# Kernel optimization log

Hardware: AMD Instinct MI355X
Metric: run time of the kernel (lower is better)

Reference implementation:

```python
import jax, jax.numpy as jnp
import numpy as np

B, S, HID = 4, 1024, 2048
NH, NKV = 32, 8
HD = HID // NH  # 64
N_REP = NH // NKV
THETA = 10000.0


def _rope_cos_sin(position_ids, head_dim, dtype):
    inv_freq = 1.0 / (THETA ** (jnp.arange(0, head_dim, 2, dtype=jnp.float32) / head_dim))
    ang = position_ids.astype(jnp.float32)[:, None] * inv_freq[None, :]  # [S, HD/2]
    emb = jnp.concatenate([ang, ang], axis=-1)  # [S, HD]
    return jnp.cos(emb).astype(dtype), jnp.sin(emb).astype(dtype)


def _rotate_half(x):
    x1, x2 = jnp.split(x, 2, axis=-1)
    return jnp.concatenate([-x2, x1], axis=-1)


def setup_inputs() -> dict:
    key = jax.random.key(0)
    ks = jax.random.split(key, 6)
    scale = 0.02
    hidden_states = jax.random.normal(ks[0], (B, S, HID), dtype=jnp.float32)
    # causal additive mask
    neg = jnp.finfo(jnp.float32).min
    causal = jnp.where(jnp.tril(jnp.ones((S, S), dtype=bool)), 0.0, neg)
    attention_mask = causal[None, None, :, :].astype(jnp.float32)
    position_ids = jnp.arange(S, dtype=jnp.int32)
    Wq = jax.random.normal(ks[1], (HID, NH * HD), dtype=jnp.float32) * scale
    Wk = jax.random.normal(ks[2], (HID, NKV * HD), dtype=jnp.float32) * scale
    Wv = jax.random.normal(ks[3], (HID, NKV * HD), dtype=jnp.float32) * scale
    Wo = jax.random.normal(ks[4], (NH * HD, HID), dtype=jnp.float32) * scale
    return {"hidden_states": hidden_states, "attention_mask": attention_mask,
            "position_ids": position_ids, "Wq": Wq, "Wk": Wk, "Wv": Wv, "Wo": Wo}


def reference(hidden_states, attention_mask, position_ids, Wq, Wk, Wv, Wo):
    b, s, _ = hidden_states.shape
    dtype = hidden_states.dtype
    q = (hidden_states @ Wq).reshape(b, s, NH, HD).transpose(0, 2, 1, 3)   # [B,NH,S,HD]
    k = (hidden_states @ Wk).reshape(b, s, NKV, HD).transpose(0, 2, 1, 3)  # [B,NKV,S,HD]
    v = (hidden_states @ Wv).reshape(b, s, NKV, HD).transpose(0, 2, 1, 3)
    # RoPE
    cos, sin = _rope_cos_sin(position_ids, HD, dtype)  # [S,HD]
    cos = cos[None, None, :, :]
    sin = sin[None, None, :, :]
    q = q * cos + _rotate_half(q) * sin
    k = k * cos + _rotate_half(k) * sin
    # repeat KV heads to match query heads
    k = jnp.repeat(k, N_REP, axis=1)  # [B,NH,S,HD]
    v = jnp.repeat(v, N_REP, axis=1)
    scale = HD ** -0.5
    attn = jnp.einsum('bhqd,bhkd->bhqk', q, k) * scale + attention_mask
    attn = jax.nn.softmax(attn.astype(jnp.float32), axis=-1).astype(dtype)
    out = jnp.einsum('bhqk,bhkd->bhqd', attn, v)  # [B,NH,S,HD]
    out = out.transpose(0, 2, 1, 3).reshape(b, s, NH * HD)
    return out @ Wo
```

## Files before the change

### kernel.cpp

```cpp
#include <hip/hip_runtime.h>
#include <hip/hip_bf16.h>
#include <math.h>

typedef __bf16 bf16_t;
typedef __bf16 bf16x4 __attribute__((ext_vector_type(4)));
typedef __bf16 bf16x8 __attribute__((ext_vector_type(8)));
typedef float f32x4 __attribute__((ext_vector_type(4)));

#define MFMA_BF16(a, b, c) __builtin_amdgcn_mfma_f32_16x16x32_bf16((a), (b), (c), 0, 0, 0)

__device__ __forceinline__ void gload_lds16(const void* g, void* s) {
  __builtin_amdgcn_global_load_lds((const __attribute__((address_space(1))) void*)g,
                                   (__attribute__((address_space(3))) void*)s, 16, 0, 0);
}

__device__ __forceinline__ bf16x8 lds_frag(const bf16_t* base, int row, int k) {
  const char* p = reinterpret_cast<const char*>(base) + row * 128 + ((((k >> 3) ^ (row & 7)) << 4));
  return *reinterpret_cast<const bf16x8*>(p);
}

__global__ __launch_bounds__(256) void k_cvt_x(const float* __restrict__ X, bf16_t* __restrict__ Xb) {
  const int i = blockIdx.x * 256 + threadIdx.x;
  const float4* X4 = reinterpret_cast<const float4*>(X);
  const float4 a = X4[2 * i], c = X4[2 * i + 1];
  bf16x8 v;
  v[0] = (bf16_t)a.x; v[1] = (bf16_t)a.y; v[2] = (bf16_t)a.z; v[3] = (bf16_t)a.w;
  v[4] = (bf16_t)c.x; v[5] = (bf16_t)c.y; v[6] = (bf16_t)c.z; v[7] = (bf16_t)c.w;
  reinterpret_cast<bf16x8*>(Xb)[i] = v;
}

__global__ __launch_bounds__(256) void k_transpose(const float* __restrict__ W, bf16_t* __restrict__ Wt,
                                                   int K, int N) {
  __shared__ bf16_t t[64][65];
  const int k0 = blockIdx.y * 64, n0 = blockIdx.x * 64;
  const int tid = threadIdx.x;
#pragma unroll
  for (int i = 0; i < 16; ++i) {
    const int idx = i * 256 + tid;
    const int kl = idx >> 6, nl = idx & 63;
    t[nl][kl] = (bf16_t)W[(size_t)(k0 + kl) * N + n0 + nl];
  }
  __syncthreads();
#pragma unroll
  for (int i = 0; i < 16; ++i) {
    const int idx = i * 256 + tid;
    const int nl = idx >> 6, kl = idx & 63;
    Wt[(size_t)(n0 + nl) * K + k0 + kl] = t[nl][kl];
  }
}

__global__ __launch_bounds__(256) void k_transpose_qkv(const float* __restrict__ Wq,
                                                       const float* __restrict__ Wk,
                                                       const float* __restrict__ Wv,
                                                       bf16_t* __restrict__ Wt) {
  __shared__ bf16_t t[64][65];
  const int n0 = blockIdx.x * 64;
  const int k0 = blockIdx.y * 64;
  const int tid = threadIdx.x;
  const float* W;
  int N, nbase;
  if (n0 < 2048)      { W = Wq; N = 2048; nbase = 0; }
  else if (n0 < 2560) { W = Wk; N = 512;  nbase = 2048; }
  else                { W = Wv; N = 512;  nbase = 2560; }
  const int nl0 = n0 - nbase;
#pragma unroll
  for (int i = 0; i < 16; ++i) {
    const int idx = i * 256 + tid;
    const int kl = idx >> 6, nl = idx & 63;
    t[nl][kl] = (bf16_t)W[(size_t)(k0 + kl) * N + nl0 + nl];
  }
  __syncthreads();
#pragma unroll
  for (int i = 0; i < 16; ++i) {
    const int idx = i * 256 + tid;
    const int nl = idx >> 6, kl = idx & 63;
    Wt[(size_t)(n0 + nl) * 2048 + k0 + kl] = t[nl][kl];
  }
}

__global__ __launch_bounds__(512) void k_gemm_qkv(const bf16_t* __restrict__ A,
                                                  const bf16_t* __restrict__ Bt,
                                                  const int* __restrict__ pos_ids,
                                                  bf16_t* __restrict__ Qb,
                                                  bf16_t* __restrict__ Kb,
                                                  bf16_t* __restrict__ Vt) {
  constexpr int K = 2048;
  constexpr int NT = K / 64;
  __shared__ __align__(16) char smem[131072];
  const int tid = threadIdx.x;
  const int w = tid >> 6, l = tid & 63;
  const int wm = w >> 2, wn = w & 3;
  const int g = l >> 4, ln = l & 15;
  const int orig = blockIdx.y * 12 + blockIdx.x;
  const int swz = (orig & 7) * 24 + (orig >> 3);
  const int m0 = (swz / 12) * 256, n0 = (swz % 12) * 256;
  const int csrc = ((l & 7) ^ (l >> 3)) * 8;
  const int srow = w * 16 + (l >> 3);

  auto STAGE_A = [&](int slot, int h, int kt) {
    char* base = smem + slot * 32768 + h * 16384 + w * 2048;
    const bf16_t* gs = A + (size_t)(m0 + h * 128 + srow) * K + kt + csrc;
    gload_lds16(gs, base);
    gload_lds16(gs + (size_t)8 * K, base + 1024);
  };
  auto STAGE_B = [&](int slot, int h, int kt) {
    char* base = smem + 65536 + slot * 32768 + h * 16384 + w * 2048;
    const bf16_t* gs = Bt + (size_t)(n0 + h * 128 + srow) * K + kt + csrc;
    gload_lds16(gs, base);
    gload_lds16(gs + (size_t)8 * K, base + 1024);
  };
  auto FRAG = [&](const char* half, int row, int kk) -> bf16x8 {
    return *reinterpret_cast<const bf16x8*>(half + row * 128 + ((((kk >> 3) ^ (row & 7)) << 4)));
  };

  const f32x4 zero4 = {0.f, 0.f, 0.f, 0.f};
  f32x4 acc[8][4];
#pragma unroll
  for (int i = 0; i < 8; ++i)
#pragma unroll
    for (int j = 0; j < 4; ++j) acc[i][j] = zero4;

  STAGE_A(0, 0, 0); STAGE_A(0, 1, 0);
  STAGE_B(0, 0, 0); STAGE_B(0, 1, 0);
  STAGE_B(1, 0, 64); STAGE_B(1, 1, 64);
  asm volatile("s_waitcnt vmcnt(4)" ::: "memory");
  __builtin_amdgcn_sched_barrier(0);
  __builtin_amdgcn_s_barrier();
  __builtin_amdgcn_sched_barrier(0);

  const int rb = (wn & 1) * 64;
  for (int t = 0; t < NT; ++t) {
    const int s = t & 1;
    const char* Ah = smem + s * 32768 + wm * 16384;
    const char* Bh = smem + 65536 + s * 32768 + (wn >> 1) * 16384;
    bf16x8 bB[4][2];
#pragma unroll
    for (int q = 0; q < 4; ++q) {
      if (q == 0) {
#pragma unroll
        for (int fc = 0; fc < 4; ++fc)
#pragma unroll
          for (int kh = 0; kh < 2; ++kh) bB[fc][kh] = FRAG(Bh, rb + fc * 16 + ln, kh * 32 + g * 8);
      }
      bf16x8 aA[2][2];
#pragma unroll
      for (int e = 0; e < 2; ++e)
#pragma unroll
        for (int kh = 0; kh < 2; ++kh) aA[e][kh] = FRAG(Ah, (q * 2 + e) * 16 + ln, kh * 32 + g * 8);
      if (q == 0 && t + 1 < NT) STAGE_A(s ^ 1, 0, (t + 1) * 64);
      if (q == 1 && t + 1 < NT) STAGE_A(s ^ 1, 1, (t + 1) * 64);
      if (q == 2 && t + 2 < NT) STAGE_B(s, 0, (t + 2) * 64);
      if (q == 3 && t + 2 < NT) STAGE_B(s, 1, (t + 2) * 64);
      if (q == 3) {
        if (t >= NT - 2) asm volatile("s_waitcnt vmcnt(0)" ::: "memory");
        else             asm volatile("s_waitcnt vmcnt(4)" ::: "memory");
      }
      __builtin_amdgcn_sched_barrier(0);
      __builtin_amdgcn_s_barrier();
      __builtin_amdgcn_sched_barrier(0);
      __builtin_amdgcn_s_setprio(1);
#pragma unroll
      for (int e = 0; e < 2; ++e)
#pragma unroll
        for (int fc = 0; fc < 4; ++fc)
#pragma unroll
          for (int kh = 0; kh < 2; ++kh)
            acc[q * 2 + e][fc] = MFMA_BF16(aA[e][kh], bB[fc][kh], acc[q * 2 + e][fc]);
      __builtin_amdgcn_s_setprio(0);
      __builtin_amdgcn_sched_barrier(0);
      __builtin_amdgcn_s_barrier();
      __builtin_amdgcn_sched_barrier(0);
    }
  }

  const int colbase = n0 + wn * 64;
  const int rowbase = m0 + wm * 128;
  const float if0 = exp2f(-(float)ln * 0.4152410118609203f);
  const float if1 = exp2f(-(float)(ln + 16) * 0.4152410118609203f);
  const float QS = 0.125f * 1.4426950408889634f;

  if (colbase < 2560) {
    const bool isQ = (colbase < 2048);
    bf16_t* out = isQ ? (Qb + (size_t)(colbase >> 6) * 1024 * 64)
                      : (Kb + (size_t)((colbase - 2048) >> 6) * 1024 * 64);
    const size_t bstride = isQ ? (size_t)32 * 1024 * 64 : (size_t)8 * 1024 * 64;
    const float sc = isQ ? QS : 1.0f;
#pragma unroll
    for (int i = 0; i < 8; ++i)
#pragma unroll
      for (int r = 0; r < 4; ++r) {
        const int row = rowbase + i * 16 + g * 4 + r;
        const int b = row >> 10, s = row & 1023;
        const float pos = (float)pos_ids[s];
        float sn0, cs0, sn1, cs1;
        __sincosf(pos * if0, &sn0, &cs0);
        __sincosf(pos * if1, &sn1, &cs1);
        const float x0 = acc[i][0][r], x1 = acc[i][1][r];
        const float x2 = acc[i][2][r], x3 = acc[i][3][r];
        const float o0 = (x0 * cs0 - x2 * sn0) * sc;
        const float o2 = (x2 * cs0 + x0 * sn0) * sc;
        const float o1 = (x1 * cs1 - x3 * sn1) * sc;
        const float o3 = (x3 * cs1 + x1 * sn1) * sc;
        bf16_t* p = out + (size_t)b * bstride + (size_t)s * 64;
        p[ln] = (bf16_t)o0;
        p[16 + ln] = (bf16_t)o1;
        p[32 + ln] = (bf16_t)o2;
        p[48 + ln] = (bf16_t)o3;
      }
  } else {
    const int kh = (colbase - 2560) >> 6;
#pragma unroll
    for (int i = 0; i < 8; ++i)
#pragma unroll
      for (int r = 0; r < 4; ++r) {
        const int row = rowbase + i * 16 + g * 4 + r;
        const int b = row >> 10, s = row & 1023;
        const size_t vb = ((size_t)(b * 8 + kh) * 64) * 1024;
#pragma unroll
        for (int j = 0; j < 4; ++j) {
          const int d = j * 16 + ln;
          Vt[vb + (size_t)d * 1024 + s] = (bf16_t)acc[i][j][r];
        }
      }
  }
}

template <typename OutT>
__global__ __launch_bounds__(256) void k_gemm(const bf16_t* __restrict__ A,
                                              const bf16_t* __restrict__ Bt,
                                              OutT* __restrict__ C,
                                              int M, int N, int K) {
  __shared__ bf16_t As[128 * 64];
  __shared__ bf16_t Bs[128 * 64];
  const int tid = threadIdx.x;
  const int w = tid >> 6, l = tid & 63;
  const int nwgx = gridDim.x;
  const int orig = blockIdx.y * nwgx + blockIdx.x;
  const int cpx = (nwgx * gridDim.y) >> 3;
  const int swz = (orig & 7) * cpx + (orig >> 3);
  const int m0 = (swz / nwgx) * 128, n0 = (swz % nwgx) * 128;
  const int wr = (w >> 1) * 64, wc = (w & 1) * 64;
  const int g = l >> 4, ln = l & 15;
  const int lr = l >> 3;
  const int csrc = ((l & 7) ^ lr) * 8;

  const f32x4 zero4 = {0.f, 0.f, 0.f, 0.f};
  f32x4 acc[4][4];
#pragma unroll
  for (int i = 0; i < 4; ++i)
#pragma unroll
    for (int j = 0; j < 4; ++j) acc[i][j] = zero4;

  for (int kt = 0; kt < K; kt += 64) {
    __syncthreads();
#pragma unroll
    for (int c = 0; c < 4; ++c) {
      const int cq = c * 4 + w;
      const int r = cq * 8 + lr;
      gload_lds16(A + (size_t)(m0 + r) * K + kt + csrc, As + cq * 512);
      gload_lds16(Bt + (size_t)(n0 + r) * K + kt + csrc, Bs + cq * 512);
    }
    asm volatile("s_waitcnt vmcnt(0)" ::: "memory");
    __syncthreads();
#pragma unroll
    for (int ks = 0; ks < 2; ++ks) {
      bf16x8 af[4], bfv[4];
#pragma unroll
      for (int i = 0; i < 4; ++i) af[i] = lds_frag(As, wr + i * 16 + ln, ks * 32 + g * 8);
#pragma unroll
      for (int j = 0; j < 4; ++j) bfv[j] = lds_frag(Bs, wc + j * 16 + ln, ks * 32 + g * 8);
#pragma unroll
      for (int i = 0; i < 4; ++i)
#pragma unroll
        for (int j = 0; j < 4; ++j) acc[i][j] = MFMA_BF16(af[i], bfv[j], acc[i][j]);
    }
  }
#pragma unroll
  for (int i = 0; i < 4; ++i)
#pragma unroll
    for (int j = 0; j < 4; ++j)
#pragma unroll
      for (int r = 0; r < 4; ++r) {
        const int row = m0 + wr + i * 16 + g * 4 + r;
        const int col = n0 + wc + j * 16 + ln;
        C[(size_t)row * N + col] = (OutT)acc[i][j][r];
      }
}

__global__ __launch_bounds__(256) void k_attn(const bf16_t* __restrict__ Qb,
                                              const bf16_t* __restrict__ Kb,
                                              const bf16_t* __restrict__ Vt,
                                              bf16_t* __restrict__ AO) {
  __shared__ bf16_t Ks[2][64 * 64];
  __shared__ bf16_t Vs[2][64 * 64];
  __shared__ bf16_t Ps[4][16 * 64];
  const int tid = threadIdx.x;
  const int w = tid >> 6, l = tid & 63;
  const int g = l >> 4, ln = l & 15;
  const int lr = l >> 3;
  const int csrc = ((l & 7) ^ lr) * 8;
  const int f = blockIdx.x;
  const int bh = blockIdx.y;
  const int b = bh >> 5, h = bh & 31, kh = h >> 2;
  const int qA0 = f * 64, qB0 = (15 - f) * 64;
  const int qAw = qA0 + w * 16, qBw = qB0 + w * 16;
  const bf16_t* Qh = Qb + (size_t)(b * 32 + h) * 1024 * 64;
  const bf16_t* Kh = Kb + (size_t)(b * 8 + kh) * 1024 * 64;
  const bf16_t* Vh = Vt + (size_t)(b * 8 + kh) * 64 * 1024;

  bf16x8 aqA[2], aqB[2];
  aqA[0] = *reinterpret_cast<const bf16x8*>(Qh + (size_t)(qAw + ln) * 64 + g * 8);
  aqA[1] = *reinterpret_cast<const bf16x8*>(Qh + (size_t)(qAw + ln) * 64 + 32 + g * 8);
  aqB[0] = *reinterpret_cast<const bf16x8*>(Qh + (size_t)(qBw + ln) * 64 + g * 8);
  aqB[1] = *reinterpret_cast<const bf16x8*>(Qh + (size_t)(qBw + ln) * 64 + 32 + g * 8);

  const f32x4 zero4 = {0.f, 0.f, 0.f, 0.f};
  f32x4 oA[4], oB[4];
#pragma unroll
  for (int d = 0; d < 4; ++d) { oA[d] = zero4; oB[d] = zero4; }
  float lA[4], lB[4];
#pragma unroll
  for (int r = 0; r < 4; ++r) { lA[r] = 0.f; lB[r] = 0.f; }

  auto STAGE = [&](int buf, int kt) {
#pragma unroll
    for (int c = 0; c < 2; ++c) {
      const int cq = c * 4 + w;
      const int r = cq * 8 + lr;
      gload_lds16(Kh + (size_t)(kt * 64 + r) * 64 + csrc, &Ks[buf][cq * 512]);
      gload_lds16(Vh + (size_t)r * 1024 + kt * 64 + csrc, &Vs[buf][cq * 512]);
    }
  };

  auto ACT = [&](const bf16x8 (&aq)[2], f32x4 (&o)[4], float (&lr_)[4],
                 int qw0, bool dg, int kt, const bf16_t* Kc, const bf16_t* Vc) {
    f32x4 sc[4];
#pragma unroll
    for (int nb = 0; nb < 4; ++nb) {
      const bf16x8 k0 = lds_frag(Kc, nb * 16 + ln, g * 8);
      const bf16x8 k1 = lds_frag(Kc, nb * 16 + ln, 32 + g * 8);
      f32x4 z = zero4;
      z = MFMA_BF16(aq[0], k0, z);
      sc[nb] = MFMA_BF16(aq[1], k1, z);
    }
#pragma unroll
    for (int r = 0; r < 4; ++r) {
      const int qrow = qw0 + g * 4 + r;
      float rs = 0.f;
#pragma unroll
      for (int nb = 0; nb < 4; ++nb) {
        float v = sc[nb][r];
        if (dg && (kt * 64 + nb * 16 + ln) > qrow) v = -INFINITY;
        const float p = exp2f(v - 16.0f);
        sc[nb][r] = p;
        rs += p;
      }
      lr_[r] += rs;
    }

    char* pw = reinterpret_cast<char*>(&Ps[w][0]);
#pragma unroll
    for (int r = 0; r < 4; ++r) {
      const int q = g * 4 + r;
      const int sw = (q & 7) << 4;
#pragma unroll
      for (int nb = 0; nb < 4; ++nb) {
        const int byte = q * 128 + ((nb * 16 + ln) * 2);
        *reinterpret_cast<bf16_t*>(pw + (byte ^ sw)) = (bf16_t)sc[nb][r];
      }
    }
    asm volatile("s_waitcnt lgkmcnt(0)" ::: "memory");

    const bf16x8 pa0 = lds_frag(&Ps[w][0], ln, g * 8);
    const bf16x8 pa1 = lds_frag(&Ps[w][0], ln, 32 + g * 8);
#pragma unroll
    for (int d = 0; d < 4; ++d) {
      const bf16x8 v0 = lds_frag(Vc, d * 16 + ln, g * 8);
      const bf16x8 v1 = lds_frag(Vc, d * 16 + ln, 32 + g * 8);
      o[d] = MFMA_BF16(pa0, v0, o[d]);
      o[d] = MFMA_BF16(pa1, v1, o[d]);
    }
  };

  const int nA = f + 1;
  STAGE(0, 0);

  for (int t = 0; t < 17; ++t) {
    const int cur = t & 1;
    asm volatile("s_waitcnt vmcnt(0)" ::: "memory");
    __syncthreads();
    if (t + 1 < 17) {
      const int ktn = (t + 1 < nA) ? (t + 1) : (t + 1 - nA);
      STAGE(cur ^ 1, ktn);
    }
    const bf16_t* Kc = &Ks[cur][0];
    const bf16_t* Vc = &Vs[cur][0];
    if (t < nA) ACT(aqA, oA, lA, qAw, t == nA - 1, t, Kc, Vc);
    else        ACT(aqB, oB, lB, qBw, t == 16, t - nA, Kc, Vc);
  }

  auto EPI = [&](f32x4 (&o)[4], float (&lr_)[4], int qw0) {
#pragma unroll
    for (int r = 0; r < 4; ++r) {
      float rs = lr_[r];
      rs += __shfl_xor(rs, 1);
      rs += __shfl_xor(rs, 2);
      rs += __shfl_xor(rs, 4);
      rs += __shfl_xor(rs, 8);
      const float inv = 1.0f / rs;
      const int srow = qw0 + g * 4 + r;
      const size_t base = ((size_t)(b * 1024 + srow)) * 2048 + h * 64;
#pragma unroll
      for (int d = 0; d < 4; ++d) AO[base + d * 16 + ln] = (bf16_t)(o[d][r] * inv);
    }
  };
  EPI(oA, lA, qAw);
  EPI(oB, lB, qBw);
}

extern "C" void kernel_launch(void* const* d_in, const int* in_sizes, int n_in,
                              void* d_out, int out_size, void* d_ws, size_t ws_size,
                              hipStream_t stream) {
  const float* X = (const float*)d_in[0];
  const int* pos = (const int*)d_in[2];
  const float* Wq = (const float*)d_in[3];
  const float* Wk = (const float*)d_in[4];
  const float* Wv = (const float*)d_in[5];
  const float* Wo = (const float*)d_in[6];
  float* out = (float*)d_out;
  char* ws = (char*)d_ws;

  bf16_t* Xb   = (bf16_t*)(ws);
  bf16_t* Wqkv = (bf16_t*)(ws + 16777216);
  bf16_t* Wot  = (bf16_t*)(ws + 29360128);
  bf16_t* Qb   = (bf16_t*)(ws + 62914560);
  bf16_t* Kb   = (bf16_t*)(ws + 79691776);
  bf16_t* Vt   = (bf16_t*)(ws + 83886080);
  bf16_t* AO   = (bf16_t*)(ws + 37748736);

  k_cvt_x<<<4096, 256, 0, stream>>>(X, Xb);
  k_transpose_qkv<<<dim3(48, 32), 256, 0, stream>>>(Wq, Wk, Wv, Wqkv);
  k_transpose<<<dim3(32, 32), 256, 0, stream>>>(Wo, Wot, 2048, 2048);
  k_gemm_qkv<<<dim3(12, 16), 512, 0, stream>>>(Xb, Wqkv, pos, Qb, Kb, Vt);
  k_attn<<<dim3(8, 128), 256, 0, stream>>>(Qb, Kb, Vt, AO);
  k_gemm<float><<<dim3(16, 32), 256, 0, stream>>>(AO, Wot, out, 4096, 2048, 2048);
}
```

Before: 180.9 us.

## Replace output-projection GEMM with pipelined 128x256 tile, 512-thread double-buffered kernel

Replaces the generic single-buffered output GEMM with a specialised kernel. It uses 128x256 tiles, 8 waves and double-buffered LDS, issuing the next A and B tile loads while the current tile's MFMAs run. Partial vmcnt waits, split barriers and setprio interleave loading with compute, which hides the global-load latency that the old waitcnt(0) per k-step exposed. The cost is more LDS (96KB), which limits occupancy to one block per CU, and only 256 blocks in the grid.

```diff
diff --git a/kernel.cpp b/kernel.cpp
--- a/kernel.cpp
+++ b/kernel.cpp
@@ -225,65 +225,107 @@
   }
 }
 
-template <typename OutT>
-__global__ __launch_bounds__(256) void k_gemm(const bf16_t* __restrict__ A,
-                                              const bf16_t* __restrict__ Bt,
-                                              OutT* __restrict__ C,
-                                              int M, int N, int K) {
-  __shared__ bf16_t As[128 * 64];
-  __shared__ bf16_t Bs[128 * 64];
+__global__ __launch_bounds__(512) void k_gemm2(const bf16_t* __restrict__ A,
+                                               const bf16_t* __restrict__ Bt,
+                                               float* __restrict__ C) {
+  constexpr int K = 2048;
+  constexpr int NT = K / 64;
+  constexpr int N = 2048;
+  __shared__ __align__(16) char smem[98304];
   const int tid = threadIdx.x;
   const int w = tid >> 6, l = tid & 63;
-  const int nwgx = gridDim.x;
-  const int orig = blockIdx.y * nwgx + blockIdx.x;
-  const int cpx = (nwgx * gridDim.y) >> 3;
-  const int swz = (orig & 7) * cpx + (orig >> 3);
-  const int m0 = (swz / nwgx) * 128, n0 = (swz % nwgx) * 128;
-  const int wr = (w >> 1) * 64, wc = (w & 1) * 64;
   const int g = l >> 4, ln = l & 15;
-  const int lr = l >> 3;
-  const int csrc = ((l & 7) ^ lr) * 8;
+  const int orig = blockIdx.y * 8 + blockIdx.x;
+  const int swz = (orig & 7) * 32 + (orig >> 3);
+  const int m0 = (swz >> 3) * 128, n0 = (swz & 7) * 256;
+  const int csrc = ((l & 7) ^ (l >> 3)) * 8;
+  const int srow = w * 16 + (l >> 3);
+
+  auto STAGE_A = [&](int slot, int kt) {
+    char* base = smem + slot * 16384 + w * 2048;
+    const bf16_t* gs = A + (size_t)(m0 + srow) * K + kt + csrc;
+    gload_lds16(gs, base);
+    gload_lds16(gs + (size_t)8 * K, base + 1024);
+  };
+  auto STAGE_B = [&](int slot, int h, int kt) {
+    char* base = smem + 32768 + slot * 32768 + h * 16384 + w * 2048;
+    const bf16_t* gs = Bt + (size_t)(n0 + h * 128 + srow) * K + kt + csrc;
+    gload_lds16(gs, base);
+    gload_lds16(gs + (size_t)8 * K, base + 1024);
+  };
+  auto FRAG = [&](const char* half, int row, int kk) -> bf16x8 {
+    return *reinterpret_cast<const bf16x8*>(half + row * 128 + ((((kk >> 3) ^ (row & 7)) << 4)));
+  };
 
   const f32x4 zero4 = {0.f, 0.f, 0.f, 0.f};
-  f32x4 acc[4][4];
-#pragma unroll
-  for (int i = 0; i < 4; ++i)
-#pragma unroll
-    for (int j = 0; j < 4; ++j) acc[i][j] = zero4;
-
-  for (int kt = 0; kt < K; kt += 64) {
-    __syncthreads();
-#pragma unroll
-    for (int c = 0; c < 4; ++c) {
-      const int cq = c * 4 + w;
-      const int r = cq * 8 + lr;
-      gload_lds16(A + (size_t)(m0 + r) * K + kt + csrc, As + cq * 512);
-      gload_lds16(Bt + (size_t)(n0 + r) * K + kt + csrc, Bs + cq * 512);
-    }
-    asm volatile("s_waitcnt vmcnt(0)" ::: "memory");
-    __syncthreads();
-#pragma unroll
-    for (int ks = 0; ks < 2; ++ks) {
-      bf16x8 af[4], bfv[4];
-#pragma unroll
-      for (int i = 0; i < 4; ++i) af[i] = lds_frag(As, wr + i * 16 + ln, ks * 32 + g * 8);
-#pragma unroll
-      for (int j = 0; j < 4; ++j) bfv[j] = lds_frag(Bs, wc + j * 16 + ln, ks * 32 + g * 8);
-#pragma unroll
-      for (int i = 0; i < 4; ++i)
-#pragma unroll
-        for (int j = 0; j < 4; ++j) acc[i][j] = MFMA_BF16(af[i], bfv[j], acc[i][j]);
-    }
-  }
-#pragma unroll
-  for (int i = 0; i < 4; ++i)
-#pragma unroll
-    for (int j = 0; j < 4; ++j)
+  f32x4 acc[8][2];
+#pragma unroll
+  for (int i = 0; i < 8; ++i)
+#pragma unroll
+    for (int j = 0; j < 2; ++j) acc[i][j] = zero4;
+
+  STAGE_A(0, 0);
+  STAGE_B(0, 0, 0); STAGE_B(0, 1, 0);
+  STAGE_B(1, 0, 64); STAGE_B(1, 1, 64);
+  asm volatile("s_waitcnt vmcnt(4)" ::: "memory");
+  __builtin_amdgcn_sched_barrier(0);
+  __builtin_amdgcn_s_barrier();
+  __builtin_amdgcn_sched_barrier(0);
+
+  const int brow = w * 32;
+  for (int t = 0; t < NT; ++t) {
+    const int s = t & 1;
+    const char* Ah = smem + s * 16384;
+    const char* Bh = smem + 32768 + s * 32768 + (brow >> 7) * 16384;
+    const int rb = brow & 127;
+    bf16x8 bB[2][2];
+#pragma unroll
+    for (int q = 0; q < 4; ++q) {
+      if (q == 0) {
+#pragma unroll
+        for (int fc = 0; fc < 2; ++fc)
+#pragma unroll
+          for (int kh = 0; kh < 2; ++kh) bB[fc][kh] = FRAG(Bh, rb + fc * 16 + ln, kh * 32 + g * 8);
+      }
+      bf16x8 aA[2][2];
+#pragma unroll
+      for (int e = 0; e < 2; ++e)
+#pragma unroll
+        for (int kh = 0; kh < 2; ++kh) aA[e][kh] = FRAG(Ah, (q * 2 + e) * 16 + ln, kh * 32 + g * 8);
+      if (q == 0 && t + 1 < NT) STAGE_A(s ^ 1, (t + 1) * 64);
+      if (q == 1 && t + 2 < NT) STAGE_B(s, 0, (t + 2) * 64);
+      if (q == 2 && t + 2 < NT) STAGE_B(s, 1, (t + 2) * 64);
+      if (q == 3) {
+        if (t >= NT - 2) asm volatile("s_waitcnt vmcnt(0)" ::: "memory");
+        else             asm volatile("s_waitcnt vmcnt(4)" ::: "memory");
+      }
+      __builtin_amdgcn_sched_barrier(0);
+      __builtin_amdgcn_s_barrier();
+      __builtin_amdgcn_sched_barrier(0);
+      __builtin_amdgcn_s_setprio(1);
+#pragma unroll
+      for (int e = 0; e < 2; ++e)
+#pragma unroll
+        for (int fc = 0; fc < 2; ++fc)
+#pragma unroll
+          for (int kh = 0; kh < 2; ++kh)
+            acc[q * 2 + e][fc] = MFMA_BF16(aA[e][kh], bB[fc][kh], acc[q * 2 + e][fc]);
+      __builtin_amdgcn_s_setprio(0);
+      __builtin_amdgcn_sched_barrier(0);
+      __builtin_amdgcn_s_barrier();
+      __builtin_amdgcn_sched_barrier(0);
+    }
+  }
+
+#pragma unroll
+  for (int i = 0; i < 8; ++i)
+#pragma unroll
+    for (int fc = 0; fc < 2; ++fc)
 #pragma unroll
       for (int r = 0; r < 4; ++r) {
-        const int row = m0 + wr + i * 16 + g * 4 + r;
-        const int col = n0 + wc + j * 16 + ln;
-        C[(size_t)row * N + col] = (OutT)acc[i][j][r];
+        const int row = m0 + i * 16 + g * 4 + r;
+        const int col = n0 + brow + fc * 16 + ln;
+        C[(size_t)row * N + col] = acc[i][fc][r];
       }
 }
 
@@ -443,5 +485,5 @@
   k_transpose<<<dim3(32, 32), 256, 0, stream>>>(Wo, Wot, 2048, 2048);
   k_gemm_qkv<<<dim3(12, 16), 512, 0, stream>>>(Xb, Wqkv, pos, Qb, Kb, Vt);
   k_attn<<<dim3(8, 128), 256, 0, stream>>>(Qb, Kb, Vt, AO);
-  k_gemm<float><<<dim3(16, 32), 256, 0, stream>>>(AO, Wot, out, 4096, 2048, 2048);
-}
+  k_gemm2<<<dim3(8, 32), 512, 0, stream>>>(AO, Wot, out);
+}
```

New measurement: 176.1 us. 1.03x faster.
